# Kernel optimization log

Measured on AMD Instinct MI355X. Metric: run time of the kernel, lower is better.

The kernel has to match this reference:

```python
import jax, jax.numpy as jnp
import numpy as np

EPS = 1e-5
KERNELS = [3, 3, 5, 7]  # 2*i+1 for i>=1, first layer k=3


def _conv_relu_bn(x, w, b, gamma, beta, rmean, rvar):
    # x: [B, Cin, S], w: [Cout, Cin, K]
    k = w.shape[-1]
    y = jax.lax.conv_general_dilated(
        x, w, window_strides=(1,), padding=[(k // 2, k // 2)],
        dimension_numbers=("NCW", "OIW", "NCW"))
    y = y + b[None, :, None]
    y = jax.nn.relu(y)
    # BatchNorm1d in inference mode (running stats)
    inv = gamma[None, :, None] / jnp.sqrt(rvar[None, :, None] + EPS)
    return (y - rmean[None, :, None]) * inv + beta[None, :, None]


def setup_inputs() -> dict:
    key = jax.random.key(0)
    ks = jax.random.split(key, 32)
    B, S = 128, 8192
    inp = {"x": jax.random.normal(ks[0], (B, 4, S), dtype=jnp.float32)}
    cin = 4
    for i, k in enumerate(KERNELS):
        inp[f"w{i}"] = jax.random.normal(ks[1 + i], (32, cin, k), dtype=jnp.float32) * 0.1
        inp[f"b{i}"] = jnp.zeros((32,), jnp.float32)
        inp[f"g{i}"] = jnp.ones((32,), jnp.float32)   # BN gamma
        inp[f"bb{i}"] = jnp.zeros((32,), jnp.float32)  # BN beta
        inp[f"rm{i}"] = jnp.zeros((32,), jnp.float32)  # running mean
        inp[f"rv{i}"] = jnp.ones((32,), jnp.float32)   # running var
        cin = 32
    inp["fw1"] = jax.random.normal(ks[10], (16, 32), dtype=jnp.float32) * 0.1
    inp["fb1"] = jnp.zeros((16,), jnp.float32)
    inp["fw2"] = jax.random.normal(ks[11], (1, 16), dtype=jnp.float32) * 0.1
    inp["fb2"] = jnp.zeros((1,), jnp.float32)
    return inp


def reference(x,
              w0, b0, g0, bb0, rm0, rv0,
              w1, b1, g1, bb1, rm1, rv1,
              w2, b2, g2, bb2, rm2, rv2,
              w3, b3, g3, bb3, rm3, rv3,
              fw1, fb1, fw2, fb2):
    x = _conv_relu_bn(x, w0, b0, g0, bb0, rm0, rv0)
    x = _conv_relu_bn(x, w1, b1, g1, bb1, rm1, rv1)
    x = _conv_relu_bn(x, w2, b2, g2, bb2, rm2, rv2)
    x = _conv_relu_bn(x, w3, b3, g3, bb3, rm3, rv3)
    # [B, 32, S] -> [B, S, 32]; the original per-timestep MLP loop is one batched GEMM
    h = jnp.einsum("bcs,hc->bsh", x, fw1) + fb1
    h = jax.nn.relu(h)  # Dropout(0.1) is identity in eval
    out = jnp.einsum("bsh,oh->bso", h, fw2) + fb2
    return out[..., 0]  # squeeze(-1) -> [B, S]
```

## Files before the change

kernel.cpp:

```cpp
#include <hip/hip_runtime.h>

#define SEQ    8192
#define S_TILE 180
#define CS     1608
#define NTHR   512
#define NREC   37
#define BN_HALFOFF (NREC*512)

typedef __attribute__((ext_vector_type(8))) _Float16 half8;
typedef __attribute__((ext_vector_type(4))) _Float16 half4v;
typedef __attribute__((ext_vector_type(4))) float    f32x4;

__device__ __forceinline__ int uni(int v){ return __builtin_amdgcn_readfirstlane(v); }

template<int K>
__device__ __forceinline__ float fold_bias(const float* __restrict__ W, int co,
    const float* __restrict__ gp, const float* __restrict__ bbp,
    const float* __restrict__ rmp, const float* __restrict__ rvp)
{
    float acc = 0.f;
#pragma unroll
    for (int ci = 0; ci < 32; ++ci) {
        float sp = gp[ci] * rsqrtf(rvp[ci] + 1e-5f);
        float tp = bbp[ci] - rmp[ci]*sp;
        float wsum = 0.f;
#pragma unroll
        for (int tap = 0; tap < K; ++tap) wsum += W[(co*32 + ci)*K + tap];
        acc += wsum * tp;
    }
    return acc;
}

extern "C" __global__ void prep_kernel(
    const float* w0, const float* w1, const float* w2, const float* w3,
    const float* b0, const float* g0, const float* bb0, const float* rm0, const float* rv0,
    const float* b1, const float* g1, const float* bb1, const float* rm1, const float* rv1,
    const float* b2, const float* g2, const float* bb2, const float* rm2, const float* rv2,
    const float* b3, const float* g3, const float* bb3, const float* rm3, const float* rv3,
    const float* fw1, const float* fb1, _Float16* ws)
{
    const int tid = threadIdx.x;
    const int rec = blockIdx.x;
    if (rec < NREC) {
        if (tid < 64) {
            const int lane = tid;
            const float* W; const float *gp = nullptr, *rvp = nullptr; int CIN, K, r2;
            if      (rec < 6)  { W = w0;  CIN = 4;  K = 3; r2 = rec;      }
            else if (rec < 12) { W = w1;  CIN = 32; K = 3; r2 = rec - 6;  gp = g0; rvp = rv0; }
            else if (rec < 22) { W = w2;  CIN = 32; K = 5; r2 = rec - 12; gp = g1; rvp = rv1; }
            else if (rec < 36) { W = w3;  CIN = 32; K = 7; r2 = rec - 22; gp = g2; rvp = rv2; }
            else               { W = fw1; CIN = 32; K = 1; r2 = 0;        gp = g3; rvp = rv3; }
            int tap = r2 >> 1, mh = r2 & 1;
            int co  = mh*16 + (lane & 15);
            int ci0 = (lane >> 4) * 8;
            half8 h;
#pragma unroll
            for (int j = 0; j < 8; ++j) {
                int ci = ci0 + j;
                float wv = (ci < CIN) ? W[(co*CIN + ci)*K + tap] : 0.0f;
                if (gp) wv *= gp[ci & 31] * rsqrtf(rvp[ci & 31] + 1e-5f);
                h[j] = (_Float16)wv;
            }
            *(half8*)(ws + rec*512 + lane*8) = h;
        }
    } else {
        float* fa = (float*)(ws + BN_HALFOFF);
        if (tid < 128) {
            int l = tid >> 5, co = tid & 31;
            const float *g, *bb, *rm, *rv, *bi;
            if      (l == 0) { g=g0; bb=bb0; rm=rm0; rv=rv0; bi=b0; }
            else if (l == 1) { g=g1; bb=bb1; rm=rm1; rv=rv1; bi=b1; }
            else if (l == 2) { g=g2; bb=bb2; rm=rm2; rv=rv2; bi=b2; }
            else             { g=g3; bb=bb3; rm=rm3; rv=rv3; bi=b3; }
            float s = g[co] * rsqrtf(rv[co] + 1e-5f);
            float t = bb[co] - rm[co]*s;
            float bias = bi[co];
            if      (l == 1) bias += fold_bias<3>(w1, co, g0, bb0, rm0, rv0);
            else if (l == 2) bias += fold_bias<5>(w2, co, g1, bb1, rm1, rv1);
            else if (l == 3) bias += fold_bias<7>(w3, co, g2, bb2, rm2, rv2);
            fa[(l*32 + co)*2 + 0] = bias;
            fa[(l*32 + co)*2 + 1] = -t / s;
        } else if (tid < 144) {
            int hh = tid - 128;
            float acc = fb1[hh];
#pragma unroll
            for (int c = 0; c < 32; ++c) {
                float s3 = g3[c] * rsqrtf(rv3[c] + 1e-5f);
                float t3 = bb3[c] - rm3[c]*s3;
                acc += fw1[hh*32 + c] * t3;
            }
            fa[256 + hh] = acc;
        }
    }
}

template<int K, int DOFF, bool BC0>
__device__ __forceinline__ void conv_layer(
    const _Float16* __restrict__ rec, const float2* __restrict__ bo,
    const _Float16* in, _Float16* outb, int s0, int ntb, int lane)
{
    const int q = lane >> 4, n = lane & 15;
    const _Float16* bbase = in + (BC0 ? 0 : q*CS) + (ntb*16 + n)*8;

    f32x4 acc[3][2];
#pragma unroll
    for (int nt = 0; nt < 3; ++nt)
#pragma unroll
        for (int mh = 0; mh < 2; ++mh) acc[nt][mh] = (f32x4){0.f, 0.f, 0.f, 0.f};

#pragma unroll
    for (int tap = 0; tap < K; ++tap) {
        half8 a0 = *(const half8*)(rec + (tap*2 + 0)*512 + lane*8);
        half8 a1 = *(const half8*)(rec + (tap*2 + 1)*512 + lane*8);
#pragma unroll
        for (int nt = 0; nt < 3; ++nt) {
            half8 bf = *(const half8*)(bbase + nt*128 + tap*8);
            acc[nt][0] = __builtin_amdgcn_mfma_f32_16x16x32_f16(a0, bf, acc[nt][0], 0, 0, 0);
            acc[nt][1] = __builtin_amdgcn_mfma_f32_16x16x32_f16(a1, bf, acc[nt][1], 0, 0, 0);
        }
    }

#pragma unroll
    for (int nt = 0; nt < 3; ++nt) {
        int pos = (ntb + nt)*16 + n;
        bool oob = (unsigned)(s0 + DOFF + pos) >= SEQ;
#pragma unroll
        for (int mh = 0; mh < 2; ++mh) {
            int co0 = mh*16 + q*4;
            half4v hv;
#pragma unroll
            for (int r = 0; r < 4; ++r) {
                float2 p = bo[co0 + r];
                float v = fmaxf(acc[nt][mh][r] + p.x, 0.0f);
                if (oob) v = p.y;
                hv[r] = (_Float16)v;
            }
            int cb = mh*2 + (q >> 1);
            *(half4v*)(outb + cb*CS + pos*8 + (q & 1)*4) = hv;
        }
    }
}

extern "C" __global__ void __launch_bounds__(NTHR, 6)
dnashape_mfma(const float* __restrict__ x, const _Float16* __restrict__ ws,
              const float* __restrict__ fw2, const float* __restrict__ fb2,
              float* __restrict__ out)
{
    __shared__ _Float16 bufA[2][4*CS];
    __shared__ _Float16 bufB[2][4*CS];

    const int tid  = threadIdx.x;
    const int tile = blockIdx.x;
    const int s0   = tile * S_TILE;
    const int b0i  = blockIdx.y * 2;

    const int lane = tid & 63;
    const int wv   = uni(tid >> 6);
    const int img  = wv >> 2;
    const int ntb  = (wv & 3) * 3;

    if (tid < 64) {
        const half8 z8 = {0,0,0,0,0,0,0,0};
        int zimg = tid >> 5, u = tid & 31;
        *(half8*)(&bufA[zimg][(u >> 3)*CS + (192 + (u & 7))*8]) = z8;
    }

    {
        const float* xb = x + (b0i + img)*4*SEQ;
        int li = ntb*16 + lane;
        if (lane < 50) {
            int sg = s0 - 7 + li;
            bool ok = (unsigned)sg < SEQ;
            float v0 = ok ? xb[0*SEQ + li + (s0 - 7) - li + sg - sg + sg - (s0-7) + (s0-7)] : 0.f;
            (void)v0;
        }
        if (lane < 50) {
            int sg = s0 - 7 + li;
            bool ok = (unsigned)sg < SEQ;
            float a0 = ok ? xb[0*SEQ + sg] : 0.f;
            float a1 = ok ? xb[1*SEQ + sg] : 0.f;
            float a2 = ok ? xb[2*SEQ + sg] : 0.f;
            float a3 = ok ? xb[3*SEQ + sg] : 0.f;
            half8 h0 = {(_Float16)a0, (_Float16)a1, (_Float16)a2, (_Float16)a3, 0, 0, 0, 0};
            *(half8*)(&bufB[img][0*CS + li*8]) = h0;
        }
    }

    const float*  fa = (const float*)(ws + BN_HALFOFF);
    const float2* bo = (const float2*)fa;

    conv_layer<3, -6, true >(ws +  0*512, bo +  0, bufB[img], bufA[img], s0, ntb, lane);
    __syncthreads();
    conv_layer<3, -5, false>(ws +  6*512, bo + 32, bufA[img], bufB[img], s0, ntb, lane);
    __syncthreads();
    conv_layer<5, -3, false>(ws + 12*512, bo + 64, bufB[img], bufA[img], s0, ntb, lane);
    __syncthreads();
    conv_layer<7,  0, false>(ws + 22*512, bo + 96, bufA[img], bufB[img], s0, ntb, lane);

    {
        const int q = lane >> 4, n = lane & 15;
        half8 am = *(const half8*)(ws + 36*512 + lane*8);
        float fb1v[4], fw2v[4];
#pragma unroll
        for (int r = 0; r < 4; ++r) { fb1v[r] = fa[256 + q*4 + r]; fw2v[r] = fw2[q*4 + r]; }
        float fb2v = fb2[0];
        const int b = b0i + img;
#pragma unroll
        for (int nt = 0; nt < 3; ++nt) {
            int pos = (ntb + nt)*16 + n;
            half8 bf = *(const half8*)(&bufB[img][q*CS + pos*8]);
            f32x4 d = {0.f, 0.f, 0.f, 0.f};
            d = __builtin_amdgcn_mfma_f32_16x16x32_f16(am, bf, d, 0, 0, 0);
            float part = 0.f;
#pragma unroll
            for (int r = 0; r < 4; ++r) part += fmaxf(d[r] + fb1v[r], 0.f)*fw2v[r];
            part += __shfl_xor(part, 16, 64);
            part += __shfl_xor(part, 32, 64);
            if (lane < 16) {
                int g = s0 + pos;
                if (pos < S_TILE && g < SEQ) out[b*SEQ + g] = part + fb2v;
            }
        }
    }
}

extern "C" void kernel_launch(void* const* d_in, const int* in_sizes, int n_in,
                              void* d_out, int out_size, void* d_ws, size_t ws_size,
                              hipStream_t stream) {
    const float* p[29];
    for (int i = 0; i < 29; ++i) p[i] = (const float*)d_in[i];
    _Float16* ws = (_Float16*)d_ws;

    prep_kernel<<<dim3(NREC + 1), 144, 0, stream>>>(
        p[1], p[7], p[13], p[19],
        p[2], p[3], p[4], p[5], p[6],
        p[8], p[9], p[10], p[11], p[12],
        p[14], p[15], p[16], p[17], p[18],
        p[20], p[21], p[22], p[23], p[24],
        p[25], p[26], ws);

    dim3 grid((SEQ + S_TILE - 1) / S_TILE, 64);
    dnashape_mfma<<<grid, NTHR, 0, stream>>>(p[0], (const _Float16*)ws,
                                             p[27], p[28], (float*)d_out);
}
```

Measured before the change: 174.8 us.

## Load conv input fragments once per layer and shift taps via DPP lane rotation

Each conv layer now loads four B-operand fragments from LDS once per wave. The per-tap shifted operands are built with DPP row-shift merges across neighbouring fragments, instead of issuing a fresh LDS read for every tap and n-tile. This cuts LDS traffic, which grows with kernel width, at the cost of extra VALU DPP ops and registers. The channel stride CS also grows, likely for padding or alignment, and the input staging drops a dead duplicate load and the lane<50 guard, so all lanes write the staging buffer.

```diff
diff --git a/kernel.cpp b/kernel.cpp
--- a/kernel.cpp
+++ b/kernel.cpp
@@ -2,7 +2,7 @@
 
 #define SEQ    8192
 #define S_TILE 180
-#define CS     1608
+#define CS     1664
 #define NTHR   512
 #define NREC   37
 #define BN_HALFOFF (NREC*512)
@@ -94,13 +94,59 @@
     }
 }
 
+template<int T>
+__device__ __forceinline__ int4 shift_merge(int4 lo, int4 hi) {
+    int4 r;
+    r.x = __builtin_amdgcn_update_dpp(0, lo.x, 0x100 + T, 0xF, 0xF, false)
+        | __builtin_amdgcn_update_dpp(0, hi.x, 0x110 + (16 - T), 0xF, 0xF, false);
+    r.y = __builtin_amdgcn_update_dpp(0, lo.y, 0x100 + T, 0xF, 0xF, false)
+        | __builtin_amdgcn_update_dpp(0, hi.y, 0x110 + (16 - T), 0xF, 0xF, false);
+    r.z = __builtin_amdgcn_update_dpp(0, lo.z, 0x100 + T, 0xF, 0xF, false)
+        | __builtin_amdgcn_update_dpp(0, hi.z, 0x110 + (16 - T), 0xF, 0xF, false);
+    r.w = __builtin_amdgcn_update_dpp(0, lo.w, 0x100 + T, 0xF, 0xF, false)
+        | __builtin_amdgcn_update_dpp(0, hi.w, 0x110 + (16 - T), 0xF, 0xF, false);
+    return r;
+}
+
+template<int K, int T>
+__device__ __forceinline__ void tap_loop(const _Float16* __restrict__ rec, int lane,
+                                         const int4 (&F)[4], f32x4 (&acc)[3][2])
+{
+    if constexpr (T < K) {
+        half8 a0 = *(const half8*)(rec + (T*2 + 0)*512 + lane*8);
+        half8 a1 = *(const half8*)(rec + (T*2 + 1)*512 + lane*8);
+        int4 d0, d1, d2;
+        if constexpr (T == 0) { d0 = F[0]; d1 = F[1]; d2 = F[2]; }
+        else {
+            d0 = shift_merge<T>(F[0], F[1]);
+            d1 = shift_merge<T>(F[1], F[2]);
+            d2 = shift_merge<T>(F[2], F[3]);
+        }
+        half8 b0 = __builtin_bit_cast(half8, d0);
+        half8 b1 = __builtin_bit_cast(half8, d1);
+        half8 b2 = __builtin_bit_cast(half8, d2);
+        acc[0][0] = __builtin_amdgcn_mfma_f32_16x16x32_f16(a0, b0, acc[0][0], 0, 0, 0);
+        acc[0][1] = __builtin_amdgcn_mfma_f32_16x16x32_f16(a1, b0, acc[0][1], 0, 0, 0);
+        acc[1][0] = __builtin_amdgcn_mfma_f32_16x16x32_f16(a0, b1, acc[1][0], 0, 0, 0);
+        acc[1][1] = __builtin_amdgcn_mfma_f32_16x16x32_f16(a1, b1, acc[1][1], 0, 0, 0);
+        acc[2][0] = __builtin_amdgcn_mfma_f32_16x16x32_f16(a0, b2, acc[2][0], 0, 0, 0);
+        acc[2][1] = __builtin_amdgcn_mfma_f32_16x16x32_f16(a1, b2, acc[2][1], 0, 0, 0);
+        tap_loop<K, T + 1>(rec, lane, F, acc);
+    }
+}
+
 template<int K, int DOFF, bool BC0>
 __device__ __forceinline__ void conv_layer(
     const _Float16* __restrict__ rec, const float2* __restrict__ bo,
     const _Float16* in, _Float16* outb, int s0, int ntb, int lane)
 {
     const int q = lane >> 4, n = lane & 15;
-    const _Float16* bbase = in + (BC0 ? 0 : q*CS) + (ntb*16 + n)*8;
+    const _Float16* bbase = in + (BC0 ? 0 : q*CS);
+
+    int4 F[4];
+#pragma unroll
+    for (int m = 0; m < 4; ++m)
+        F[m] = *(const int4*)(bbase + ((ntb + m)*16 + n)*8);
 
     f32x4 acc[3][2];
 #pragma unroll
@@ -108,17 +154,7 @@
 #pragma unroll
         for (int mh = 0; mh < 2; ++mh) acc[nt][mh] = (f32x4){0.f, 0.f, 0.f, 0.f};
 
-#pragma unroll
-    for (int tap = 0; tap < K; ++tap) {
-        half8 a0 = *(const half8*)(rec + (tap*2 + 0)*512 + lane*8);
-        half8 a1 = *(const half8*)(rec + (tap*2 + 1)*512 + lane*8);
-#pragma unroll
-        for (int nt = 0; nt < 3; ++nt) {
-            half8 bf = *(const half8*)(bbase + nt*128 + tap*8);
-            acc[nt][0] = __builtin_amdgcn_mfma_f32_16x16x32_f16(a0, bf, acc[nt][0], 0, 0, 0);
-            acc[nt][1] = __builtin_amdgcn_mfma_f32_16x16x32_f16(a1, bf, acc[nt][1], 0, 0, 0);
-        }
-    }
+    tap_loop<K, 0>(rec, lane, F, acc);
 
 #pragma unroll
     for (int nt = 0; nt < 3; ++nt) {
@@ -168,22 +204,14 @@
     {
         const float* xb = x + (b0i + img)*4*SEQ;
         int li = ntb*16 + lane;
-        if (lane < 50) {
-            int sg = s0 - 7 + li;
-            bool ok = (unsigned)sg < SEQ;
-            float v0 = ok ? xb[0*SEQ + li + (s0 - 7) - li + sg - sg + sg - (s0-7) + (s0-7)] : 0.f;
-            (void)v0;
-        }
-        if (lane < 50) {
-            int sg = s0 - 7 + li;
-            bool ok = (unsigned)sg < SEQ;
-            float a0 = ok ? xb[0*SEQ + sg] : 0.f;
-            float a1 = ok ? xb[1*SEQ + sg] : 0.f;
-            float a2 = ok ? xb[2*SEQ + sg] : 0.f;
-            float a3 = ok ? xb[3*SEQ + sg] : 0.f;
-            half8 h0 = {(_Float16)a0, (_Float16)a1, (_Float16)a2, (_Float16)a3, 0, 0, 0, 0};
-            *(half8*)(&bufB[img][0*CS + li*8]) = h0;
-        }
+        int sg = s0 - 7 + li;
+        bool ok = (unsigned)sg < SEQ;
+        float a0 = ok ? xb[0*SEQ + sg] : 0.f;
+        float a1 = ok ? xb[1*SEQ + sg] : 0.f;
+        float a2 = ok ? xb[2*SEQ + sg] : 0.f;
+        float a3 = ok ? xb[3*SEQ + sg] : 0.f;
+        half8 h0 = {(_Float16)a0, (_Float16)a1, (_Float16)a2, (_Float16)a3, 0, 0, 0, 0};
+        *(half8*)(&bufB[img][0*CS + li*8]) = h0;
     }
 
     const float*  fa = (const float*)(ws + BN_HALFOFF);
```

New measurement: 176.1 us. No clear change (+0.8%).
